# Kernel optimization log

Hardware: AMD Instinct MI355X
Metric: run time of the kernel (lower is better)

Reference implementation:

```python
import jax, jax.numpy as jnp
import numpy as np

N, E, D, B = 50000, 800000, 64, 64
NEXP, NC, EDIM, PDIM = 4, 10, 4, 100


def setup_inputs() -> dict:
    key = jax.random.key(0)
    ks = jax.random.split(key, 24)
    s = lambda f: 1.0 / np.sqrt(f)
    inp = {
        'x': jax.random.normal(ks[0], (N, D), jnp.float32),
        'edge_index': jax.random.randint(ks[1], (2, E), 0, N, jnp.int32),
        'edge_attr': jax.random.normal(ks[2], (E, EDIM), jnp.float32),
        'batch': jnp.sort(jax.random.randint(ks[3], (N,), 0, B, jnp.int32)),
        'ldxb_flag': jax.random.normal(ks[4], (B,), jnp.float32),
        # layer 1 params
        'w_edge1': jax.random.normal(ks[5], (D, EDIM)) * s(EDIM),
        'b_edge1': jnp.zeros((D,), jnp.float32),
        'w_ih1': jax.random.normal(ks[6], (3 * D, D)) * s(D),
        'w_hh1': jax.random.normal(ks[7], (3 * D, D)) * s(D),
        'b_ih1': jnp.zeros((3 * D,), jnp.float32),
        'b_hh1': jnp.zeros((3 * D,), jnp.float32),
        # layer 2 params
        'w_edge2': jax.random.normal(ks[8], (D, EDIM)) * s(EDIM),
        'b_edge2': jnp.zeros((D,), jnp.float32),
        'w_ih2': jax.random.normal(ks[9], (3 * D, D)) * s(D),
        'w_hh2': jax.random.normal(ks[10], (3 * D, D)) * s(D),
        'b_ih2': jnp.zeros((3 * D,), jnp.float32),
        'b_hh2': jnp.zeros((3 * D,), jnp.float32),
        # MoE
        'gate_w': jax.random.normal(ks[11], (NEXP, D)) * s(D),
        'gate_b': jnp.zeros((NEXP,), jnp.float32),
        'exp_w': jax.random.normal(ks[12], (NEXP, D, D)) * s(D),
        'exp_b': jnp.zeros((NEXP, D), jnp.float32),
        # heads
        'proj_w': jax.random.normal(ks[13], (PDIM, 1)),
        'proj_b': jnp.zeros((PDIM,), jnp.float32),
        'fc_w': jax.random.normal(ks[14], (NC, D + PDIM)) * s(D + PDIM),
        'fc_b': jnp.zeros((NC,), jnp.float32),
    }
    return inp


def _ggnn_layer(x, src, dst, eemb, w_ih, w_hh, b_ih, b_hh):
    # gather + scatter-add message passing (self-loops already in src/dst/eemb)
    msg = x[src] + eemb                       # [E+N, D]
    m = jnp.zeros_like(x).at[dst].add(msg)    # [N, D]
    # GRUCell(m, x): x is the hidden state
    gi = m @ w_ih.T + b_ih
    gh = x @ w_hh.T + b_hh
    i_r, i_z, i_n = jnp.split(gi, 3, axis=1)
    h_r, h_z, h_n = jnp.split(gh, 3, axis=1)
    r = jax.nn.sigmoid(i_r + h_r)
    z = jax.nn.sigmoid(i_z + h_z)
    n = jnp.tanh(i_n + r * h_n)
    return (1.0 - z) * n + z * x


def reference(x, edge_index, edge_attr, batch, ldxb_flag,
              w_edge1, b_edge1, w_ih1, w_hh1, b_ih1, b_hh1,
              w_edge2, b_edge2, w_ih2, w_hh2, b_ih2, b_hh2,
              gate_w, gate_b, exp_w, exp_b, proj_w, proj_b, fc_w, fc_b):
    n = x.shape[0]
    loop = jnp.arange(n, dtype=edge_index.dtype)
    src = jnp.concatenate([edge_index[0], loop])
    dst = jnp.concatenate([edge_index[1], loop])
    ea = jnp.concatenate([edge_attr, jnp.zeros((n, edge_attr.shape[1]), edge_attr.dtype)], axis=0)

    h = _ggnn_layer(x, src, dst, ea @ w_edge1.T + b_edge1, w_ih1, w_hh1, b_ih1, b_hh1)
    h = jax.nn.relu(h)
    h = _ggnn_layer(h, src, dst, ea @ w_edge2.T + b_edge2, w_ih2, w_hh2, b_ih2, b_hh2)
    h = jax.nn.relu(h)

    # soft MoE combine
    gw = jax.nn.softmax(h @ gate_w.T + gate_b, axis=1)            # [N, NEXP]
    eo = jax.nn.relu(jnp.einsum('nd,ehd->neh', h, exp_w) + exp_b)  # [N, NEXP, D]
    h = jnp.einsum('ne,neh->nh', gw, eo)                           # [N, D]

    # global mean pool per graph
    sums = jax.ops.segment_sum(h, batch, num_segments=B)
    cnts = jax.ops.segment_sum(jnp.ones((n,), h.dtype), batch, num_segments=B)
    graph_emb = sums / jnp.maximum(cnts, 1.0)[:, None]             # [B, D]

    flag = ldxb_flag[:, None] @ proj_w.T + proj_b                  # [B, 100]
    logits = jnp.concatenate([flag, graph_emb], axis=1) @ fc_w.T + fc_b
    return (graph_emb, graph_emb, logits)
```

## Files before the change

kernel.cpp:

```cpp
#include <hip/hip_runtime.h>
#include <stdint.h>


#define SUBCAP 8
#define OVF_MAX 32768
#define PS 16

typedef __bf16 bf16x8 __attribute__((ext_vector_type(8)));
typedef float floatx4 __attribute__((ext_vector_type(4)));
typedef unsigned short us8 __attribute__((ext_vector_type(8)));

__device__ __forceinline__ unsigned short f2bf(float f){
  union { float f; unsigned u; } c; c.f = f;
  unsigned r = c.u + 0x7FFFu + ((c.u >> 16) & 1u);
  return (unsigned short)(r >> 16);
}
__device__ __forceinline__ float bf2f(unsigned short u){
  union { unsigned u; float f; } c; c.u = ((unsigned)u) << 16; return c.f;
}
__device__ __forceinline__ float sigm(float x){ return 1.f/(1.f + __expf(-x)); }

__global__ void k_init(const float* __restrict__ s0, const float* __restrict__ s1,
                       const float* __restrict__ s2, const float* __restrict__ s3,
                       const float* __restrict__ s4, const float* __restrict__ s5,
                       unsigned short* __restrict__ dst,
                       int* __restrict__ cur, int* __restrict__ ovfcnt, int N8){
  int i = blockIdx.x*blockDim.x + threadIdx.x;
  if (i < N8) cur[i] = 0;
  if (i == 0){ ovfcnt[0] = 0; }
  if (i >= 65792) return;
  const float* s; int off;
  if      (i < 12288){ s = s0; off = i; }
  else if (i < 24576){ s = s1; off = i - 12288; }
  else if (i < 36864){ s = s2; off = i - 24576; }
  else if (i < 49152){ s = s3; off = i - 36864; }
  else if (i < 49408){ s = s4; off = i - 49152; }
  else               { s = s5; off = i - 49408; }
  dst[i] = f2bf(s[off]);
}

__global__ void k_bucket(const int* __restrict__ ei, const float* __restrict__ ea,
                         int* __restrict__ cur, int* __restrict__ bkt_src,
                         ushort4* __restrict__ bkt_ea,
                         int* __restrict__ ovfcnt, int* __restrict__ ovf,
                         int E, int N){
  int e = blockIdx.x*blockDim.x + threadIdx.x;
  if (e >= E) return;
  int sub = blockIdx.x & 7;
  int s = ei[e];
  int d = ei[E + e];
  size_t sb = (size_t)sub*N + d;
  int pos = atomicAdd(&cur[sb], 1);
  if (pos < SUBCAP){
    float4 v = *(const float4*)(ea + (size_t)e*4);
    ushort4 p; p.x = f2bf(v.x); p.y = f2bf(v.y); p.z = f2bf(v.z); p.w = f2bf(v.w);
    bkt_src[sb*SUBCAP + pos] = s;
    bkt_ea [sb*SUBCAP + pos] = p;
  } else {
    int o = atomicAdd(ovfcnt, 1);
    if (o < OVF_MAX) ovf[o] = e;
  }
}

__global__ void __launch_bounds__(256) k_gather(
    const int* __restrict__ cur, const int* __restrict__ bkt_src,
    const ushort4* __restrict__ bkt_ea,
    const float* __restrict__ xin,
    const float* __restrict__ w_edge, const float* __restrict__ b_edge,
    float* __restrict__ m, int N){
  int n = (int)(((long long)blockIdx.x*blockDim.x + threadIdx.x) >> 6);
  if (n >= N) return;
  int d = threadIdx.x & 63;
  int sub = d >> 3, k = d & 7;
  size_t sb = (size_t)sub*N + n;
  int myc = cur[sb];
  int contrib = (k == 0) ? myc : 0;
#pragma unroll
  for (int off = 1; off < 64; off <<= 1) contrib += __shfl_xor(contrib, off);
  int degAll = contrib;

  bool valid = k < min(myc, SUBCAP);
  int src = 0;
  float esx = 0.f, esy = 0.f, esz = 0.f, esw = 0.f;
  if (valid){
    src = bkt_src[sb*SUBCAP + k];
    ushort4 p = bkt_ea[sb*SUBCAP + k];
    esx = bf2f(p.x); esy = bf2f(p.y); esz = bf2f(p.z); esw = bf2f(p.w);
  }

  float4 wv = *(const float4*)(w_edge + d*4);
  float acc = xin[(size_t)n*64 + d] + (float)(degAll + 1) * b_edge[d];

  unsigned long long mm = __ballot(valid);
  while (mm){
    int l0 = (int)__builtin_ctzll(mm); mm &= mm - 1;
    int s0 = __shfl(src, l0);
    float a0 = xin[(size_t)s0*64 + d];
    float a1 = 0.f, a2 = 0.f, a3 = 0.f;
    if (mm){
      int l1 = (int)__builtin_ctzll(mm); mm &= mm - 1;
      int s1 = __shfl(src, l1);
      a1 = xin[(size_t)s1*64 + d];
      if (mm){
        int l2 = (int)__builtin_ctzll(mm); mm &= mm - 1;
        int s2 = __shfl(src, l2);
        a2 = xin[(size_t)s2*64 + d];
        if (mm){
          int l3 = (int)__builtin_ctzll(mm); mm &= mm - 1;
          int s3 = __shfl(src, l3);
          a3 = xin[(size_t)s3*64 + d];
        }
      }
    }
    acc += (a0 + a1) + (a2 + a3);
  }

#pragma unroll
  for (int off = 1; off < 64; off <<= 1){
    esx += __shfl_xor(esx, off);
    esy += __shfl_xor(esy, off);
    esz += __shfl_xor(esz, off);
    esw += __shfl_xor(esw, off);
  }
  acc += esx*wv.x + esy*wv.y + esz*wv.z + esw*wv.w;
  m[(size_t)n*64 + d] = acc;
}

__global__ void k_ovf(const int* __restrict__ ei, const float* __restrict__ ea,
                      const float* __restrict__ xin, const float* __restrict__ w_edge,
                      const int* __restrict__ ovf, const int* __restrict__ ovfcnt,
                      float* __restrict__ m, int E){
  int cnt = *ovfcnt; if (cnt > OVF_MAX) cnt = OVF_MAX;
  int nwaves = (gridDim.x * blockDim.x) >> 6;
  int wid = (int)((blockIdx.x*blockDim.x + threadIdx.x) >> 6);
  int d = threadIdx.x & 63;
  for (int k = wid; k < cnt; k += nwaves){
    int e = ovf[k];
    int s = ei[e], dst = ei[E + e];
    float4 v  = *(const float4*)(ea + (size_t)e*4);
    float4 wv = *(const float4*)(w_edge + d*4);
    float msg = xin[(size_t)s*64 + d] + v.x*wv.x + v.y*wv.y + v.z*wv.z + v.w*wv.w;
    atomicAdd(&m[(size_t)dst*64 + d], msg);
  }
}

__global__ void __launch_bounds__(256) k_gru(
    const float* __restrict__ m, const float* x,
    const unsigned short* __restrict__ wih, const unsigned short* __restrict__ whh,
    const float* __restrict__ b_ih, const float* __restrict__ b_hh,
    float* out, int tiles, int N){
  int wid = (int)(((long long)blockIdx.x*blockDim.x + threadIdx.x) >> 6);
  if (wid >= tiles) return;
  int lane = threadIdx.x & 63;
  int col = lane & 15, quad = lane >> 4;
  int na = wid*16 + col; if (na > N-1) na = N-1;

  bf16x8 am[2], ax[2];
#pragma unroll
  for (int ks = 0; ks < 2; ++ks){
    int kb = ks*32 + quad*8;
    const float4* mp = (const float4*)(m + (size_t)na*64 + kb);
    float4 lo = mp[0], hi = mp[1];
    us8 tm;
    tm[0]=f2bf(lo.x); tm[1]=f2bf(lo.y); tm[2]=f2bf(lo.z); tm[3]=f2bf(lo.w);
    tm[4]=f2bf(hi.x); tm[5]=f2bf(hi.y); tm[6]=f2bf(hi.z); tm[7]=f2bf(hi.w);
    am[ks] = __builtin_bit_cast(bf16x8, tm);
    const float4* xp = (const float4*)(x + (size_t)na*64 + kb);
    float4 xlo = xp[0], xhi = xp[1];
    us8 tx;
    tx[0]=f2bf(xlo.x); tx[1]=f2bf(xlo.y); tx[2]=f2bf(xlo.z); tx[3]=f2bf(xlo.w);
    tx[4]=f2bf(xhi.x); tx[5]=f2bf(xhi.y); tx[6]=f2bf(xhi.z); tx[7]=f2bf(xhi.w);
    ax[ks] = __builtin_bit_cast(bf16x8, tx);
  }

  floatx4 ai[12], ah[12];
#pragma unroll
  for (int nt = 0; nt < 12; ++nt){ ai[nt] = (floatx4)0.f; ah[nt] = (floatx4)0.f; }
#pragma unroll
  for (int nt = 0; nt < 12; ++nt){
    int r = nt*16 + col;
#pragma unroll
    for (int ks = 0; ks < 2; ++ks){
      int kb = ks*32 + quad*8;
      bf16x8 bi = __builtin_bit_cast(bf16x8, *(const us8*)(wih + (size_t)r*64 + kb));
      ai[nt] = __builtin_amdgcn_mfma_f32_16x16x32_bf16(am[ks], bi, ai[nt], 0,0,0);
      bf16x8 bh = __builtin_bit_cast(bf16x8, *(const us8*)(whh + (size_t)r*64 + kb));
      ah[nt] = __builtin_amdgcn_mfma_f32_16x16x32_bf16(ax[ks], bh, ah[nt], 0,0,0);
    }
  }

#pragma unroll
  for (int nt = 0; nt < 4; ++nt){
    int d = nt*16 + col;
    float bir = b_ih[d],      bhr = b_hh[d];
    float biz = b_ih[64+d],   bhz = b_hh[64+d];
    float bin = b_ih[128+d],  bhn = b_hh[128+d];
#pragma unroll
    for (int rg = 0; rg < 4; ++rg){
      int node = wid*16 + quad*4 + rg;
      if (node >= N) continue;
      float rr = sigm(ai[nt  ][rg] + bir + ah[nt  ][rg] + bhr);
      float zz = sigm(ai[nt+4][rg] + biz + ah[nt+4][rg] + bhz);
      float nn = tanhf(ai[nt+8][rg] + bin + rr*(ah[nt+8][rg] + bhn));
      float xv = x[(size_t)node*64 + d];
      float hv = (1.f - zz)*nn + zz*xv;
      out[(size_t)node*64 + d] = fmaxf(hv, 0.f);
    }
  }
}

__global__ void __launch_bounds__(256) k_moe(
    const float* __restrict__ h,
    const unsigned short* __restrict__ gate_w, const float* __restrict__ gate_b,
    const unsigned short* __restrict__ exp_w,  const float* __restrict__ exp_b,
    float* __restrict__ v_out, int tiles, int N){
  __shared__ float gsm[4][16][4];
  int gwid = (int)(((long long)blockIdx.x*blockDim.x + threadIdx.x) >> 6);
  int w = threadIdx.x >> 6;
  int lane = threadIdx.x & 63;
  int col = lane & 15, quad = lane >> 4;
  bool active = gwid < tiles;

  floatx4 accg = (floatx4)0.f;
  floatx4 acce[4][4];
#pragma unroll
  for (int e=0;e<4;++e)
#pragma unroll
    for (int nt=0;nt<4;++nt) acce[e][nt] = (floatx4)0.f;

  if (active){
    int na = gwid*16 + col; if (na > N-1) na = N-1;
    bf16x8 a[2];
#pragma unroll
    for (int ks=0; ks<2; ++ks){
      int kb = ks*32 + quad*8;
      const float4* hp = (const float4*)(h + (size_t)na*64 + kb);
      float4 lo = hp[0], hi = hp[1];
      us8 th;
      th[0]=f2bf(lo.x); th[1]=f2bf(lo.y); th[2]=f2bf(lo.z); th[3]=f2bf(lo.w);
      th[4]=f2bf(hi.x); th[5]=f2bf(hi.y); th[6]=f2bf(hi.z); th[7]=f2bf(hi.w);
      a[ks] = __builtin_bit_cast(bf16x8, th);
      us8 braw = {0,0,0,0,0,0,0,0};
      if (col < 4) braw = *(const us8*)(gate_w + col*64 + kb);
      accg = __builtin_amdgcn_mfma_f32_16x16x32_bf16(a[ks], __builtin_bit_cast(bf16x8, braw), accg, 0,0,0);
    }
#pragma unroll
    for (int e=0;e<4;++e)
#pragma unroll
      for (int nt=0;nt<4;++nt)
#pragma unroll
        for (int ks=0;ks<2;++ks){
          int kb = ks*32 + quad*8;
          bf16x8 b = __builtin_bit_cast(bf16x8,
              *(const us8*)(exp_w + ((size_t)e*64 + nt*16 + col)*64 + kb));
          acce[e][nt] = __builtin_amdgcn_mfma_f32_16x16x32_bf16(a[ks], b, acce[e][nt], 0,0,0);
        }
    if (col < 4){
      float gb = gate_b[col];
#pragma unroll
      for (int rg=0;rg<4;++rg) gsm[w][quad*4+rg][col] = accg[rg] + gb;
    }
  }
  __syncthreads();
  if (!active) return;

#pragma unroll
  for (int rg=0; rg<4; ++rg){
    int nrow = quad*4 + rg;
    int node = gwid*16 + nrow;
    if (node >= N) continue;
    float g0=gsm[w][nrow][0], g1=gsm[w][nrow][1], g2=gsm[w][nrow][2], g3=gsm[w][nrow][3];
    float mx = fmaxf(fmaxf(g0,g1), fmaxf(g2,g3));
    float e0=__expf(g0-mx), e1=__expf(g1-mx), e2=__expf(g2-mx), e3=__expf(g3-mx);
    float inv = 1.f/(e0+e1+e2+e3);
    float w0=e0*inv, w1=e1*inv, w2=e2*inv, w3=e3*inv;
#pragma unroll
    for (int nt=0;nt<4;++nt){
      int o = nt*16 + col;
      float v = w0*fmaxf(acce[0][nt][rg] + exp_b[      o], 0.f)
              + w1*fmaxf(acce[1][nt][rg] + exp_b[ 64 + o], 0.f)
              + w2*fmaxf(acce[2][nt][rg] + exp_b[128 + o], 0.f)
              + w3*fmaxf(acce[3][nt][rg] + exp_b[192 + o], 0.f);
      v_out[(size_t)node*64 + o] = v;
    }
  }
}

__device__ __forceinline__ int lower_bound_i(const int* __restrict__ a, int n, int key){
  int lo = 0, hi = n;
  while (lo < hi){ int mid = (lo + hi) >> 1; if (a[mid] < key) lo = mid + 1; else hi = mid; }
  return lo;
}

__global__ void __launch_bounds__(256) k_pool(
    const float* __restrict__ v, const int* __restrict__ batch, int N,
    float* __restrict__ partial){
  __shared__ float red[4][64];
  int g = blockIdx.x / PS, s = blockIdx.x % PS;
  int t = threadIdx.x, d = t & 63, r = t >> 6;
  int start = lower_bound_i(batch, N, g);
  int end   = lower_bound_i(batch, N, g + 1);
  int len = end - start;
  int per = (len + PS - 1) / PS;
  int s0 = start + s*per;
  int s1 = s0 + per; if (s1 > end) s1 = end;
  float acc = 0.f;
  for (int i = s0 + r; i < s1; i += 4)
    acc += v[(size_t)i*64 + d];
  red[r][d] = acc;
  __syncthreads();
  if (r == 0)
    partial[(size_t)blockIdx.x*64 + d] = red[0][d] + red[1][d] + red[2][d] + red[3][d];
}

__global__ void __launch_bounds__(64) k_head(
    const float* __restrict__ partial, const int* __restrict__ batch, int N, int B,
    const float* __restrict__ ldxb,
    const float* __restrict__ proj_w, const float* __restrict__ proj_b,
    const float* __restrict__ fc_w, const float* __restrict__ fc_b,
    float* __restrict__ out){
  __shared__ float ges[64];
  int b = blockIdx.x, d = threadIdx.x;
  int start = lower_bound_i(batch, N, b);
  int end   = lower_bound_i(batch, N, b + 1);
  float sum = 0.f;
#pragma unroll
  for (int s = 0; s < PS; ++s)
    sum += partial[((size_t)b*PS + s)*64 + d];
  float ge = sum / fmaxf((float)(end - start), 1.f);
  ges[d] = ge;
  out[(size_t)b*64 + d]                = ge;
  out[(size_t)B*64 + (size_t)b*64 + d] = ge;
  __syncthreads();
  if (d < 10){
    float acc = fc_b[d];
    float fl = ldxb[b];
    const float* fr = fc_w + d*164;
    for (int p = 0; p < 100; ++p) acc += (fl*proj_w[p] + proj_b[p]) * fr[p];
    for (int dd = 0; dd < 64; ++dd) acc += ges[dd]*fr[100 + dd];
    out[(size_t)B*128 + (size_t)b*10 + d] = acc;
  }
}

extern "C" void kernel_launch(void* const* d_in, const int* in_sizes, int n_in,
                              void* d_out, int out_size, void* d_ws, size_t ws_size,
                              hipStream_t stream){
  const float* x      = (const float*)d_in[0];
  const int*   ei     = (const int*)d_in[1];
  const float* ea     = (const float*)d_in[2];
  const int*   batch  = (const int*)d_in[3];
  const float* ldxb   = (const float*)d_in[4];
  const float* w_edge1= (const float*)d_in[5];
  const float* b_edge1= (const float*)d_in[6];
  const float* w_ih1  = (const float*)d_in[7];
  const float* w_hh1  = (const float*)d_in[8];
  const float* b_ih1  = (const float*)d_in[9];
  const float* b_hh1  = (const float*)d_in[10];
  const float* w_edge2= (const float*)d_in[11];
  const float* b_edge2= (const float*)d_in[12];
  const float* w_ih2  = (const float*)d_in[13];
  const float* w_hh2  = (const float*)d_in[14];
  const float* b_ih2  = (const float*)d_in[15];
  const float* b_hh2  = (const float*)d_in[16];
  const float* gate_w = (const float*)d_in[17];
  const float* gate_b = (const float*)d_in[18];
  const float* exp_w  = (const float*)d_in[19];
  const float* exp_b  = (const float*)d_in[20];
  const float* proj_w = (const float*)d_in[21];
  const float* proj_b = (const float*)d_in[22];
  const float* fc_w   = (const float*)d_in[23];
  const float* fc_b   = (const float*)d_in[24];
  float* out = (float*)d_out;

  int N = in_sizes[0] / 64;
  int E = in_sizes[1] / 2;
  int B = in_sizes[4];
  int tiles = (N + 15) / 16;
  int nTot = N * 64;

  float*   m       = (float*)d_ws;
  float*   h       = m + (size_t)nTot;
  int*     bkt_src = (int*)(h + (size_t)nTot);
  ushort4* bkt_ea  = (ushort4*)(bkt_src + (size_t)nTot);
  int*     cur     = (int*)(bkt_ea + (size_t)nTot);
  int*     ovfcnt  = cur + (size_t)N*8;
  int*     ovf     = ovfcnt + 4;
  unsigned short* wbf = (unsigned short*)(ovf + OVF_MAX);
  float*   partial = (float*)(wbf + 65792);
  unsigned short* wih1bf = wbf;
  unsigned short* whh1bf = wbf + 12288;
  unsigned short* wih2bf = wbf + 24576;
  unsigned short* whh2bf = wbf + 36864;
  unsigned short* gatebf = wbf + 49152;
  unsigned short* expbf  = wbf + 49408;

  dim3 blk(256);
  int edgeBlocks = (E + 255)/256;
  int nodeWaveBlocks = (N + 3)/4;
  int waveBlocks = (tiles + 3)/4;
  int N8 = N*8;
  int initBlocks = ((N8 > 65792 ? N8 : 65792) + 255)/256;

  k_init<<<initBlocks, blk, 0, stream>>>(w_ih1, w_hh1, w_ih2, w_hh2, gate_w, exp_w,
                                         wbf, cur, ovfcnt, N8);
  k_bucket<<<edgeBlocks, blk, 0, stream>>>(ei, ea, cur, bkt_src, bkt_ea, ovfcnt, ovf, E, N);
  k_gather<<<nodeWaveBlocks, blk, 0, stream>>>(cur, bkt_src, bkt_ea, x, w_edge1, b_edge1, m, N);
  k_ovf<<<8, blk, 0, stream>>>(ei, ea, x, w_edge1, ovf, ovfcnt, m, E);
  k_gru<<<waveBlocks, blk, 0, stream>>>(m, x, wih1bf, whh1bf, b_ih1, b_hh1, h, tiles, N);
  k_gather<<<nodeWaveBlocks, blk, 0, stream>>>(cur, bkt_src, bkt_ea, h, w_edge2, b_edge2, m, N);
  k_ovf<<<8, blk, 0, stream>>>(ei, ea, h, w_edge2, ovf, ovfcnt, m, E);
  k_gru<<<waveBlocks, blk, 0, stream>>>(m, h, wih2bf, whh2bf, b_ih2, b_hh2, h, tiles, N);
  k_moe<<<waveBlocks, blk, 0, stream>>>(h, gatebf, gate_b, expbf, exp_b, m, tiles, N);
  k_pool<<<B*PS, blk, 0, stream>>>(m, batch, N, partial);
  k_head<<<B, 64, 0, stream>>>(partial, batch, N, B, ldxb, proj_w, proj_b, fc_w, fc_b, out);
}
```

Measured before the change: 365.6 us.

## Fuse second GRU layer with MoE, pack bucket records, shrink bucket capacity

Merges the second GRU kernel and the MoE kernel into one kernel. The GRU output for each 16-node tile is staged in shared memory and fed straight into the gate and expert MFMAs, so the hidden state is never written to or re-read from global memory. Each edge's source index and bf16 edge attributes are now packed into a single int4 record so the gather does one vector load instead of two. Bucket capacity drops from 8 to 6, and the overflow kernel gets more blocks to absorb the extra spilled edges. The trade-offs are more overflow edges going through the slower atomic path, plus higher register and shared-memory use in the fused kernel.

```diff
diff --git a/kernel.cpp b/kernel.cpp
--- a/kernel.cpp
+++ b/kernel.cpp
@@ -2,7 +2,7 @@
 #include <stdint.h>
 
 
-#define SUBCAP 8
+#define SUBCAP 6
 #define OVF_MAX 32768
 #define PS 16
 
@@ -40,8 +40,7 @@
 }
 
 __global__ void k_bucket(const int* __restrict__ ei, const float* __restrict__ ea,
-                         int* __restrict__ cur, int* __restrict__ bkt_src,
-                         ushort4* __restrict__ bkt_ea,
+                         int* __restrict__ cur, int4* __restrict__ bkt,
                          int* __restrict__ ovfcnt, int* __restrict__ ovf,
                          int E, int N){
   int e = blockIdx.x*blockDim.x + threadIdx.x;
@@ -53,9 +52,12 @@
   int pos = atomicAdd(&cur[sb], 1);
   if (pos < SUBCAP){
     float4 v = *(const float4*)(ea + (size_t)e*4);
-    ushort4 p; p.x = f2bf(v.x); p.y = f2bf(v.y); p.z = f2bf(v.z); p.w = f2bf(v.w);
-    bkt_src[sb*SUBCAP + pos] = s;
-    bkt_ea [sb*SUBCAP + pos] = p;
+    int4 rec;
+    rec.x = s;
+    rec.y = (int)((unsigned)f2bf(v.x) | ((unsigned)f2bf(v.y) << 16));
+    rec.z = (int)((unsigned)f2bf(v.z) | ((unsigned)f2bf(v.w) << 16));
+    rec.w = 0;
+    bkt[sb*SUBCAP + pos] = rec;
   } else {
     int o = atomicAdd(ovfcnt, 1);
     if (o < OVF_MAX) ovf[o] = e;
@@ -63,8 +65,7 @@
 }
 
 __global__ void __launch_bounds__(256) k_gather(
-    const int* __restrict__ cur, const int* __restrict__ bkt_src,
-    const ushort4* __restrict__ bkt_ea,
+    const int* __restrict__ cur, const int4* __restrict__ bkt,
     const float* __restrict__ xin,
     const float* __restrict__ w_edge, const float* __restrict__ b_edge,
     float* __restrict__ m, int N){
@@ -83,9 +84,12 @@
   int src = 0;
   float esx = 0.f, esy = 0.f, esz = 0.f, esw = 0.f;
   if (valid){
-    src = bkt_src[sb*SUBCAP + k];
-    ushort4 p = bkt_ea[sb*SUBCAP + k];
-    esx = bf2f(p.x); esy = bf2f(p.y); esz = bf2f(p.z); esw = bf2f(p.w);
+    int4 rec = bkt[sb*SUBCAP + k];
+    src = rec.x;
+    esx = bf2f((unsigned short)(rec.y      ));
+    esy = bf2f((unsigned short)(rec.y >> 16));
+    esz = bf2f((unsigned short)(rec.z      ));
+    esw = bf2f((unsigned short)(rec.z >> 16));
   }
 
   float4 wv = *(const float4*)(w_edge + d*4);
@@ -209,17 +213,92 @@
   }
 }
 
-__global__ void __launch_bounds__(256) k_moe(
-    const float* __restrict__ h,
+__global__ void __launch_bounds__(256) k_gru_moe(
+    const float* __restrict__ m, const float* __restrict__ x,
+    const unsigned short* __restrict__ wih, const unsigned short* __restrict__ whh,
+    const float* __restrict__ b_ih, const float* __restrict__ b_hh,
     const unsigned short* __restrict__ gate_w, const float* __restrict__ gate_b,
     const unsigned short* __restrict__ exp_w,  const float* __restrict__ exp_b,
     float* __restrict__ v_out, int tiles, int N){
+  __shared__ float hs[4][16][68];
   __shared__ float gsm[4][16][4];
-  int gwid = (int)(((long long)blockIdx.x*blockDim.x + threadIdx.x) >> 6);
+  int wid = (int)(((long long)blockIdx.x*blockDim.x + threadIdx.x) >> 6);
   int w = threadIdx.x >> 6;
   int lane = threadIdx.x & 63;
   int col = lane & 15, quad = lane >> 4;
-  bool active = gwid < tiles;
+  bool active = wid < tiles;
+
+  if (active){
+    int na = wid*16 + col; if (na > N-1) na = N-1;
+    bf16x8 am[2], ax[2];
+#pragma unroll
+    for (int ks = 0; ks < 2; ++ks){
+      int kb = ks*32 + quad*8;
+      const float4* mp = (const float4*)(m + (size_t)na*64 + kb);
+      float4 lo = mp[0], hi = mp[1];
+      us8 tm;
+      tm[0]=f2bf(lo.x); tm[1]=f2bf(lo.y); tm[2]=f2bf(lo.z); tm[3]=f2bf(lo.w);
+      tm[4]=f2bf(hi.x); tm[5]=f2bf(hi.y); tm[6]=f2bf(hi.z); tm[7]=f2bf(hi.w);
+      am[ks] = __builtin_bit_cast(bf16x8, tm);
+      const float4* xp = (const float4*)(x + (size_t)na*64 + kb);
+      float4 xlo = xp[0], xhi = xp[1];
+      us8 tx;
+      tx[0]=f2bf(xlo.x); tx[1]=f2bf(xlo.y); tx[2]=f2bf(xlo.z); tx[3]=f2bf(xlo.w);
+      tx[4]=f2bf(xhi.x); tx[5]=f2bf(xhi.y); tx[6]=f2bf(xhi.z); tx[7]=f2bf(xhi.w);
+      ax[ks] = __builtin_bit_cast(bf16x8, tx);
+    }
+
+    floatx4 ai[12], ah[12];
+#pragma unroll
+    for (int nt = 0; nt < 12; ++nt){ ai[nt] = (floatx4)0.f; ah[nt] = (floatx4)0.f; }
+#pragma unroll
+    for (int nt = 0; nt < 12; ++nt){
+      int r = nt*16 + col;
+#pragma unroll
+      for (int ks = 0; ks < 2; ++ks){
+        int kb = ks*32 + quad*8;
+        bf16x8 bi = __builtin_bit_cast(bf16x8, *(const us8*)(wih + (size_t)r*64 + kb));
+        ai[nt] = __builtin_amdgcn_mfma_f32_16x16x32_bf16(am[ks], bi, ai[nt], 0,0,0);
+        bf16x8 bh = __builtin_bit_cast(bf16x8, *(const us8*)(whh + (size_t)r*64 + kb));
+        ah[nt] = __builtin_amdgcn_mfma_f32_16x16x32_bf16(ax[ks], bh, ah[nt], 0,0,0);
+      }
+    }
+
+#pragma unroll
+    for (int nt = 0; nt < 4; ++nt){
+      int d = nt*16 + col;
+      float bir = b_ih[d],      bhr = b_hh[d];
+      float biz = b_ih[64+d],   bhz = b_hh[64+d];
+      float bin = b_ih[128+d],  bhn = b_hh[128+d];
+#pragma unroll
+      for (int rg = 0; rg < 4; ++rg){
+        int node = wid*16 + quad*4 + rg;
+        float hv = 0.f;
+        if (node < N){
+          float rr = sigm(ai[nt  ][rg] + bir + ah[nt  ][rg] + bhr);
+          float zz = sigm(ai[nt+4][rg] + biz + ah[nt+4][rg] + bhz);
+          float nn = tanhf(ai[nt+8][rg] + bin + rr*(ah[nt+8][rg] + bhn));
+          float xv = x[(size_t)node*64 + d];
+          hv = fmaxf((1.f - zz)*nn + zz*xv, 0.f);
+        }
+        hs[w][quad*4 + rg][d] = hv;
+      }
+    }
+  }
+  __syncthreads();
+  if (!active) return;
+
+  bf16x8 a[2];
+#pragma unroll
+  for (int ks = 0; ks < 2; ++ks){
+    int kb = ks*32 + quad*8;
+    const float4* hp = (const float4*)&hs[w][col][kb];
+    float4 lo = hp[0], hi = hp[1];
+    us8 th;
+    th[0]=f2bf(lo.x); th[1]=f2bf(lo.y); th[2]=f2bf(lo.z); th[3]=f2bf(lo.w);
+    th[4]=f2bf(hi.x); th[5]=f2bf(hi.y); th[6]=f2bf(hi.z); th[7]=f2bf(hi.w);
+    a[ks] = __builtin_bit_cast(bf16x8, th);
+  }
 
   floatx4 accg = (floatx4)0.f;
   floatx4 acce[4][4];
@@ -228,46 +307,34 @@
 #pragma unroll
     for (int nt=0;nt<4;++nt) acce[e][nt] = (floatx4)0.f;
 
-  if (active){
-    int na = gwid*16 + col; if (na > N-1) na = N-1;
-    bf16x8 a[2];
-#pragma unroll
-    for (int ks=0; ks<2; ++ks){
-      int kb = ks*32 + quad*8;
-      const float4* hp = (const float4*)(h + (size_t)na*64 + kb);
-      float4 lo = hp[0], hi = hp[1];
-      us8 th;
-      th[0]=f2bf(lo.x); th[1]=f2bf(lo.y); th[2]=f2bf(lo.z); th[3]=f2bf(lo.w);
-      th[4]=f2bf(hi.x); th[5]=f2bf(hi.y); th[6]=f2bf(hi.z); th[7]=f2bf(hi.w);
-      a[ks] = __builtin_bit_cast(bf16x8, th);
-      us8 braw = {0,0,0,0,0,0,0,0};
-      if (col < 4) braw = *(const us8*)(gate_w + col*64 + kb);
-      accg = __builtin_amdgcn_mfma_f32_16x16x32_bf16(a[ks], __builtin_bit_cast(bf16x8, braw), accg, 0,0,0);
-    }
-#pragma unroll
-    for (int e=0;e<4;++e)
-#pragma unroll
-      for (int nt=0;nt<4;++nt)
-#pragma unroll
-        for (int ks=0;ks<2;++ks){
-          int kb = ks*32 + quad*8;
-          bf16x8 b = __builtin_bit_cast(bf16x8,
-              *(const us8*)(exp_w + ((size_t)e*64 + nt*16 + col)*64 + kb));
-          acce[e][nt] = __builtin_amdgcn_mfma_f32_16x16x32_bf16(a[ks], b, acce[e][nt], 0,0,0);
-        }
-    if (col < 4){
-      float gb = gate_b[col];
-#pragma unroll
-      for (int rg=0;rg<4;++rg) gsm[w][quad*4+rg][col] = accg[rg] + gb;
-    }
-  }
-  __syncthreads();
-  if (!active) return;
+#pragma unroll
+  for (int ks=0; ks<2; ++ks){
+    int kb = ks*32 + quad*8;
+    us8 braw = {0,0,0,0,0,0,0,0};
+    if (col < 4) braw = *(const us8*)(gate_w + col*64 + kb);
+    accg = __builtin_amdgcn_mfma_f32_16x16x32_bf16(a[ks], __builtin_bit_cast(bf16x8, braw), accg, 0,0,0);
+  }
+#pragma unroll
+  for (int e=0;e<4;++e)
+#pragma unroll
+    for (int nt=0;nt<4;++nt)
+#pragma unroll
+      for (int ks=0;ks<2;++ks){
+        int kb = ks*32 + quad*8;
+        bf16x8 b = __builtin_bit_cast(bf16x8,
+            *(const us8*)(exp_w + ((size_t)e*64 + nt*16 + col)*64 + kb));
+        acce[e][nt] = __builtin_amdgcn_mfma_f32_16x16x32_bf16(a[ks], b, acce[e][nt], 0,0,0);
+      }
+  if (col < 4){
+    float gb = gate_b[col];
+#pragma unroll
+    for (int rg=0;rg<4;++rg) gsm[w][quad*4+rg][col] = accg[rg] + gb;
+  }
 
 #pragma unroll
   for (int rg=0; rg<4; ++rg){
     int nrow = quad*4 + rg;
-    int node = gwid*16 + nrow;
+    int node = wid*16 + nrow;
     if (node >= N) continue;
     float g0=gsm[w][nrow][0], g1=gsm[w][nrow][1], g2=gsm[w][nrow][2], g3=gsm[w][nrow][3];
     float mx = fmaxf(fmaxf(g0,g1), fmaxf(g2,g3));
@@ -380,9 +447,8 @@
 
   float*   m       = (float*)d_ws;
   float*   h       = m + (size_t)nTot;
-  int*     bkt_src = (int*)(h + (size_t)nTot);
-  ushort4* bkt_ea  = (ushort4*)(bkt_src + (size_t)nTot);
-  int*     cur     = (int*)(bkt_ea + (size_t)nTot);
+  int4*    bkt     = (int4*)(h + (size_t)nTot);
+  int*     cur     = (int*)(bkt + (size_t)N*8*SUBCAP);
   int*     ovfcnt  = cur + (size_t)N*8;
   int*     ovf     = ovfcnt + 4;
   unsigned short* wbf = (unsigned short*)(ovf + OVF_MAX);
@@ -403,14 +469,14 @@
 
   k_init<<<initBlocks, blk, 0, stream>>>(w_ih1, w_hh1, w_ih2, w_hh2, gate_w, exp_w,
                                          wbf, cur, ovfcnt, N8);
-  k_bucket<<<edgeBlocks, blk, 0, stream>>>(ei, ea, cur, bkt_src, bkt_ea, ovfcnt, ovf, E, N);
-  k_gather<<<nodeWaveBlocks, blk, 0, stream>>>(cur, bkt_src, bkt_ea, x, w_edge1, b_edge1, m, N);
-  k_ovf<<<8, blk, 0, stream>>>(ei, ea, x, w_edge1, ovf, ovfcnt, m, E);
+  k_bucket<<<edgeBlocks, blk, 0, stream>>>(ei, ea, cur, bkt, ovfcnt, ovf, E, N);
+  k_gather<<<nodeWaveBlocks, blk, 0, stream>>>(cur, bkt, x, w_edge1, b_edge1, m, N);
+  k_ovf<<<64, blk, 0, stream>>>(ei, ea, x, w_edge1, ovf, ovfcnt, m, E);
   k_gru<<<waveBlocks, blk, 0, stream>>>(m, x, wih1bf, whh1bf, b_ih1, b_hh1, h, tiles, N);
-  k_gather<<<nodeWaveBlocks, blk, 0, stream>>>(cur, bkt_src, bkt_ea, h, w_edge2, b_edge2, m, N);
-  k_ovf<<<8, blk, 0, stream>>>(ei, ea, h, w_edge2, ovf, ovfcnt, m, E);
-  k_gru<<<waveBlocks, blk, 0, stream>>>(m, h, wih2bf, whh2bf, b_ih2, b_hh2, h, tiles, N);
-  k_moe<<<waveBlocks, blk, 0, stream>>>(h, gatebf, gate_b, expbf, exp_b, m, tiles, N);
+  k_gather<<<nodeWaveBlocks, blk, 0, stream>>>(cur, bkt, h, w_edge2, b_edge2, m, N);
+  k_ovf<<<64, blk, 0, stream>>>(ei, ea, h, w_edge2, ovf, ovfcnt, m, E);
+  k_gru_moe<<<waveBlocks, blk, 0, stream>>>(m, h, wih2bf, whh2bf, b_ih2, b_hh2,
+                                            gatebf, gate_b, expbf, exp_b, m, tiles, N);
   k_pool<<<B*PS, blk, 0, stream>>>(m, batch, N, partial);
   k_head<<<B, 64, 0, stream>>>(partial, batch, N, B, ldxb, proj_w, proj_b, fc_w, fc_b, out);
 }
```

Result: slower. 378.3 us (+3.5%).

## Pack edge buckets into 16-byte records and process two edges per thread

Applied to the files above, without the earlier changes.

Merges the separate source-index and bf16 edge-attribute bucket arrays into one interleaved int4 record per edge, so gather reads one 16-byte load per slot. The bucket kernel now handles two edges per thread with vectorized index loads, and per-subbucket capacity drops from 8 to 6. Overflow kernels get more blocks to absorb the larger overflow count from the smaller capacity. The risk is that overflow edges are handled by slower atomic scatter, and the 4-byte padding slot wastes bandwidth.

```diff
diff --git a/kernel.cpp b/kernel.cpp
--- a/kernel.cpp
+++ b/kernel.cpp
@@ -2,7 +2,7 @@
 #include <stdint.h>
 
 
-#define SUBCAP 8
+#define SUBCAP 6
 #define OVF_MAX 32768
 #define PS 16
 
@@ -40,31 +40,50 @@
 }
 
 __global__ void k_bucket(const int* __restrict__ ei, const float* __restrict__ ea,
-                         int* __restrict__ cur, int* __restrict__ bkt_src,
-                         ushort4* __restrict__ bkt_ea,
+                         int* __restrict__ cur, int4* __restrict__ bkt,
                          int* __restrict__ ovfcnt, int* __restrict__ ovf,
                          int E, int N){
-  int e = blockIdx.x*blockDim.x + threadIdx.x;
-  if (e >= E) return;
+  int base = (blockIdx.x*blockDim.x + threadIdx.x)*2;
+  if (base >= E) return;
   int sub = blockIdx.x & 7;
-  int s = ei[e];
-  int d = ei[E + e];
-  size_t sb = (size_t)sub*N + d;
-  int pos = atomicAdd(&cur[sb], 1);
-  if (pos < SUBCAP){
-    float4 v = *(const float4*)(ea + (size_t)e*4);
-    ushort4 p; p.x = f2bf(v.x); p.y = f2bf(v.y); p.z = f2bf(v.z); p.w = f2bf(v.w);
-    bkt_src[sb*SUBCAP + pos] = s;
-    bkt_ea [sb*SUBCAP + pos] = p;
+  bool v1 = base + 1 < E;
+  int2 ss = *(const int2*)(ei + base);
+  int2 dd = *(const int2*)(ei + E + base);
+  if (!v1){ dd.y = dd.x; ss.y = ss.x; }
+  float4 a0 = *(const float4*)(ea + (size_t)base*4);
+  float4 a1 = v1 ? *(const float4*)(ea + (size_t)(base+1)*4) : a0;
+  size_t sb0 = (size_t)sub*N + dd.x;
+  size_t sb1 = (size_t)sub*N + dd.y;
+  int p0 = atomicAdd(&cur[sb0], 1);
+  int p1 = v1 ? atomicAdd(&cur[sb1], 1) : SUBCAP;
+  if (p0 < SUBCAP){
+    int4 rec;
+    rec.x = ss.x;
+    rec.y = (int)((unsigned)f2bf(a0.x) | ((unsigned)f2bf(a0.y) << 16));
+    rec.z = (int)((unsigned)f2bf(a0.z) | ((unsigned)f2bf(a0.w) << 16));
+    rec.w = 0;
+    bkt[sb0*SUBCAP + p0] = rec;
   } else {
     int o = atomicAdd(ovfcnt, 1);
-    if (o < OVF_MAX) ovf[o] = e;
+    if (o < OVF_MAX) ovf[o] = base;
+  }
+  if (v1){
+    if (p1 < SUBCAP){
+      int4 rec;
+      rec.x = ss.y;
+      rec.y = (int)((unsigned)f2bf(a1.x) | ((unsigned)f2bf(a1.y) << 16));
+      rec.z = (int)((unsigned)f2bf(a1.z) | ((unsigned)f2bf(a1.w) << 16));
+      rec.w = 0;
+      bkt[sb1*SUBCAP + p1] = rec;
+    } else {
+      int o = atomicAdd(ovfcnt, 1);
+      if (o < OVF_MAX) ovf[o] = base + 1;
+    }
   }
 }
 
 __global__ void __launch_bounds__(256) k_gather(
-    const int* __restrict__ cur, const int* __restrict__ bkt_src,
-    const ushort4* __restrict__ bkt_ea,
+    const int* __restrict__ cur, const int4* __restrict__ bkt,
     const float* __restrict__ xin,
     const float* __restrict__ w_edge, const float* __restrict__ b_edge,
     float* __restrict__ m, int N){
@@ -83,9 +102,12 @@
   int src = 0;
   float esx = 0.f, esy = 0.f, esz = 0.f, esw = 0.f;
   if (valid){
-    src = bkt_src[sb*SUBCAP + k];
-    ushort4 p = bkt_ea[sb*SUBCAP + k];
-    esx = bf2f(p.x); esy = bf2f(p.y); esz = bf2f(p.z); esw = bf2f(p.w);
+    int4 rec = bkt[sb*SUBCAP + k];
+    src = rec.x;
+    esx = bf2f((unsigned short)(rec.y      ));
+    esy = bf2f((unsigned short)(rec.y >> 16));
+    esz = bf2f((unsigned short)(rec.z      ));
+    esw = bf2f((unsigned short)(rec.z >> 16));
   }
 
   float4 wv = *(const float4*)(w_edge + d*4);
@@ -380,9 +402,8 @@
 
   float*   m       = (float*)d_ws;
   float*   h       = m + (size_t)nTot;
-  int*     bkt_src = (int*)(h + (size_t)nTot);
-  ushort4* bkt_ea  = (ushort4*)(bkt_src + (size_t)nTot);
-  int*     cur     = (int*)(bkt_ea + (size_t)nTot);
+  int4*    bkt     = (int4*)(h + (size_t)nTot);
+  int*     cur     = (int*)(bkt + (size_t)N*8*SUBCAP);
   int*     ovfcnt  = cur + (size_t)N*8;
   int*     ovf     = ovfcnt + 4;
   unsigned short* wbf = (unsigned short*)(ovf + OVF_MAX);
@@ -395,7 +416,7 @@
   unsigned short* expbf  = wbf + 49408;
 
   dim3 blk(256);
-  int edgeBlocks = (E + 255)/256;
+  int edgePairBlocks = (((E + 1)/2) + 255)/256;
   int nodeWaveBlocks = (N + 3)/4;
   int waveBlocks = (tiles + 3)/4;
   int N8 = N*8;
@@ -403,12 +424,12 @@
 
   k_init<<<initBlocks, blk, 0, stream>>>(w_ih1, w_hh1, w_ih2, w_hh2, gate_w, exp_w,
                                          wbf, cur, ovfcnt, N8);
-  k_bucket<<<edgeBlocks, blk, 0, stream>>>(ei, ea, cur, bkt_src, bkt_ea, ovfcnt, ovf, E, N);
-  k_gather<<<nodeWaveBlocks, blk, 0, stream>>>(cur, bkt_src, bkt_ea, x, w_edge1, b_edge1, m, N);
-  k_ovf<<<8, blk, 0, stream>>>(ei, ea, x, w_edge1, ovf, ovfcnt, m, E);
+  k_bucket<<<edgePairBlocks, blk, 0, stream>>>(ei, ea, cur, bkt, ovfcnt, ovf, E, N);
+  k_gather<<<nodeWaveBlocks, blk, 0, stream>>>(cur, bkt, x, w_edge1, b_edge1, m, N);
+  k_ovf<<<64, blk, 0, stream>>>(ei, ea, x, w_edge1, ovf, ovfcnt, m, E);
   k_gru<<<waveBlocks, blk, 0, stream>>>(m, x, wih1bf, whh1bf, b_ih1, b_hh1, h, tiles, N);
-  k_gather<<<nodeWaveBlocks, blk, 0, stream>>>(cur, bkt_src, bkt_ea, h, w_edge2, b_edge2, m, N);
-  k_ovf<<<8, blk, 0, stream>>>(ei, ea, h, w_edge2, ovf, ovfcnt, m, E);
+  k_gather<<<nodeWaveBlocks, blk, 0, stream>>>(cur, bkt, h, w_edge2, b_edge2, m, N);
+  k_ovf<<<64, blk, 0, stream>>>(ei, ea, h, w_edge2, ovf, ovfcnt, m, E);
   k_gru<<<waveBlocks, blk, 0, stream>>>(m, h, wih2bf, whh2bf, b_ih2, b_hh2, h, tiles, N);
   k_moe<<<waveBlocks, blk, 0, stream>>>(h, gatebf, gate_b, expbf, exp_b, m, tiles, N);
   k_pool<<<B*PS, blk, 0, stream>>>(m, batch, N, partial);
```

New measurement: 385.6 us. 5.5% more time.
